# Kernel tuning notes

Measured on AMD Instinct MI355X. Metric: run time of the kernel, lower is better.

The kernel has to match this reference:

```python
import jax, jax.numpy as jnp
import numpy as np

EPS = 1e-5
GRID = (16, 16)
BLOCK = (16, 16)


def _ln(x):
    # LayerNorm over (C, H, W) per sample, affine = identity (fresh nn.LayerNorm each call)
    m = jnp.mean(x, axis=(1, 2, 3), keepdims=True)
    v = jnp.mean(jnp.square(x - m), axis=(1, 2, 3), keepdims=True)
    return (x - m) / jnp.sqrt(v + EPS)


def _gelu(x):
    return jax.nn.gelu(x, approximate=False)  # torch F.gelu default = exact erf


def _block(x, fh, fw):
    # NCHW -> [N, C, gh*gw, fh*fw]
    n, c, h, w = x.shape
    gh, gw = h // fh, w // fw
    return x.reshape(n, c, gh, fh, gw, fw).transpose(0, 1, 2, 4, 3, 5).reshape(n, c, gh * gw, fh * fw)


def _unblock(x, gh, gw, fh, fw):
    n, c, _, _ = x.shape
    return x.reshape(n, c, gh, gw, fh, fw).transpose(0, 1, 2, 4, 3, 5).reshape(n, c, gh * fh, gw * fw)


def _gating(x, w1, b1, w2, b2, w3, b3, w4, b4):
    # GetSpatialGatingWeights
    n, c, h, w = x.shape
    x = _ln(x)
    x = jnp.einsum('nchw,cd->ndhw', x, w1) + b1[None, :, None, None]  # C -> 2C
    x = _gelu(x)
    u, v = jnp.split(x, 2, axis=1)
    # grid MLP on u: mix across gh*gw grid positions
    gh, gw = GRID
    fh, fw = h // gh, w // gw
    u = _block(u, fh, fw)                                             # [n,c,G,P]
    u = jnp.einsum('ncgp,gd->ncdp', u, w2) + b2[None, None, :, None]
    u = _unblock(u, gh, gw, fh, fw)
    # block MLP on v: mix across fh*fw positions inside each block
    fh, fw = BLOCK
    gh, gw = h // fh, w // fw
    v = _block(v, fh, fw)
    v = jnp.einsum('ncgp,pd->ncgd', v, w3) + b3
    v = _unblock(v, gh, gw, fh, fw)
    x = jnp.concatenate([u, v], axis=1)
    return jnp.einsum('nchw,cd->ndhw', x, w4) + b4[None, :, None, None]  # 2C -> C


def _chan_lin(x, w, b):
    return jnp.einsum('nchw,cd->ndhw', x, w) + b[None, :, None, None]


def setup_inputs() -> dict:
    key = jax.random.key(0)
    ks = list(jax.random.split(key, 40))
    k = iter(ks)

    def rn(shape, s=0.02):
        return jax.random.normal(next(k), shape, dtype=jnp.float32) * s

    N, Cx, Cy, F, H, W = 8, 128, 256, 128, 128, 128
    G = GRID[0] * GRID[1]    # 256
    B = BLOCK[0] * BLOCK[1]  # 256
    inp = {
        'x': jax.random.normal(next(k), (N, Cx, H, W), dtype=jnp.float32),
        'y': jax.random.normal(next(k), (N, Cy, H // 2, W // 2), dtype=jnp.float32),
        'wt': rn((Cy, F, 2, 2)), 'bt': rn((F,)),
        'wc1': rn((Cx, F)), 'bc1': rn((F,)),
        'wc2': rn((F, F)), 'bc2': rn((F,)),
        'wl1': rn((F, F)), 'bl1': rn((F,)),
        'wl2': rn((F, F)), 'bl2': rn((F,)),
        'wl3': rn((F, F)), 'bl3': rn((F,)),
        'wl4': rn((F, F)), 'bl4': rn((F,)),
    }
    for p in ('g1', 'g2'):
        inp[p + '_w1'] = rn((F, 2 * F)); inp[p + '_b1'] = rn((2 * F,))
        inp[p + '_w2'] = rn((G, G));     inp[p + '_b2'] = rn((G,))
        inp[p + '_w3'] = rn((B, B));     inp[p + '_b3'] = rn((B,))
        inp[p + '_w4'] = rn((2 * F, F)); inp[p + '_b4'] = rn((F,))
    return inp


def reference(x, y, wt, bt, wc1, bc1, wc2, bc2, wl1, bl1, wl2, bl2, wl3, bl3, wl4, bl4,
              g1_w1, g1_b1, g1_w2, g1_b2, g1_w3, g1_b3, g1_w4, g1_b4,
              g2_w1, g2_b1, g2_w2, g2_b2, g2_w3, g2_b3, g2_w4, g2_b4):
    # ConvT_up: kernel=2, stride=2 (non-overlapping) + ReLU
    n, cy, hy, wy = y.shape
    fo = wt.shape[1]
    y = jnp.einsum('nchw,cokl->nohkwl', y, wt).reshape(n, fo, 2 * hy, 2 * wy) + bt[None, :, None, None]
    y = jax.nn.relu(y)
    # Conv1x1 (+ReLU) projections
    x = jax.nn.relu(_chan_lin(x, wc1, bc1))
    y = jax.nn.relu(_chan_lin(y, wc2, bc2))
    shortcut_x, shortcut_y = x, y
    # x branch
    x = _gelu(_chan_lin(_ln(x), wl1, bl1))
    gx = _gating(x, g1_w1, g1_b1, g1_w2, g1_b2, g1_w3, g1_b3, g1_w4, g1_b4)
    # y branch
    y = _gelu(_chan_lin(_ln(y), wl2, bl2))
    gy = _gating(y, g2_w1, g2_b1, g2_w2, g2_b2, g2_w3, g2_b3, g2_w4, g2_b4)
    # cross gating + residuals (dropout p=0.0 -> identity)
    y = _chan_lin(y * gx, wl3, bl3) + shortcut_y
    x = _chan_lin(x * gy, wl4, bl4) + y + shortcut_x
    return x, y
```

## Files before the change

### kernel.cpp

```cpp
#include <hip/hip_runtime.h>
#include <hip/hip_bf16.h>


typedef unsigned short u16;
typedef __bf16 bf16x8 __attribute__((ext_vector_type(8)));
typedef u16    u16x8  __attribute__((ext_vector_type(8)));
typedef u16    u16x4  __attribute__((ext_vector_type(4)));
typedef float  f32x4  __attribute__((ext_vector_type(4)));

__device__ __forceinline__ float bf2f(u16 u) {
  union { float f; unsigned int i; } v; v.i = ((unsigned int)u) << 16; return v.f;
}
__device__ __forceinline__ u16 f2bf(float f) {
  union { float f; unsigned int i; } v; v.f = f;
  unsigned int x = v.i;
  return (u16)((x + 0x7fffu + ((x >> 16) & 1u)) >> 16);
}
__device__ __forceinline__ f32x4 mfma16(u16x8 a, u16x8 b, f32x4 c) {
  return __builtin_amdgcn_mfma_f32_16x16x32_bf16(
      __builtin_bit_cast(bf16x8, a), __builtin_bit_cast(bf16x8, b), c, 0, 0, 0);
}
__device__ __forceinline__ float gelu_erf(float v) {
  return 0.5f * v * (1.0f + erff(v * 0.70710678118654752f));
}

__global__ __launch_bounds__(256) void prep_k(
    const float* __restrict__ wc1f, const float* __restrict__ wc2f,
    const float* __restrict__ wl1f, const float* __restrict__ wl2f,
    const float* __restrict__ wl3f, const float* __restrict__ wl4f,
    const float* __restrict__ g1w1, const float* __restrict__ g2w1,
    const float* __restrict__ g1w4, const float* __restrict__ g2w4,
    const float* __restrict__ g1w2, const float* __restrict__ g2w2,
    const float* __restrict__ g1w3, const float* __restrict__ g2w3,
    const float* __restrict__ wtf,
    u16* __restrict__ wb, float* __restrict__ cs, float* __restrict__ ps) {
  const int b = blockIdx.x, t = threadIdx.x;
  if (b < 384) {
    const float* src = b < 64 ? wc1f : b < 128 ? wc2f : b < 192 ? wl1f
                     : b < 256 ? wl2f : b < 320 ? wl3f : wl4f;
    const int w = b >> 6;
    const int i = ((b & 63) << 8) + t;
    const int d = i >> 7, c = i & 127;
    wb[w * 16384 + i] = f2bf(src[c * 128 + d]);
  } else if (b < 640) {
    const float* src = b < 512 ? g1w1 : g2w1;
    const int base = b < 512 ? 98304 : 131072;
    const int i = (((b - (b < 512 ? 384 : 512)) << 8) + t);
    const int d = i >> 7, c = i & 127;
    wb[base + i] = f2bf(src[c * 256 + d]);
  } else if (b < 896) {
    const float* src = b < 768 ? g1w4 : g2w4;
    const int base = b < 768 ? 163840 : 196608;
    const int i = (((b - (b < 768 ? 640 : 768)) << 8) + t);
    const int d = i >> 8, c = i & 255;
    wb[base + i] = f2bf(src[c * 128 + d]);
  } else if (b < 1920) {
    const int w = (b - 896) >> 8;
    const float* src = w == 0 ? g1w2 : w == 1 ? g2w2 : w == 2 ? g1w3 : g2w3;
    const int base = 229376 + w * 65536;
    const int i = (((b - 896) & 255) << 8) + t;
    const int d = i >> 8, g = i & 255;
    wb[base + i] = f2bf(src[g * 256 + d]);
  } else if (b < 2432) {
    const int i = ((b - 1920) << 8) + t;
    const int c = i & 255, r = i >> 8, o = r & 127, kl = r >> 7;
    wb[491520 + i] = f2bf(wtf[(c * 128 + o) * 4 + kl]);
  } else if (b < 2436) {
    const int w = b - 2432;
    const float* src = w == 0 ? wl1f : w == 1 ? wl2f : w == 2 ? g1w1 : g2w1;
    const int cout = w < 2 ? 128 : 256;
    if (t < cout) {
      float s = 0.f;
      for (int c = 0; c < 128; ++c) s += bf2f(f2bf(src[c * cout + t]));
      cs[w * 256 + t] = s;
    }
  } else {
    if (t < 64) ps[t] = 0.f;
  }
}

__global__ __launch_bounds__(256, 2) void gemmX_k(
    const float* __restrict__ X, const u16* __restrict__ Wt,
    const float* __restrict__ bias, u16* __restrict__ out,
    float* __restrict__ pso) {
  __shared__ u16 As[128 * 136];
  __shared__ float red[8];
  const int tid = threadIdx.x;
  const int m0 = blockIdx.x * 128;
  const int ns = m0 >> 14, pb = m0 & 16383;
  const int wid = tid >> 6, lane = tid & 63, fr = lane & 15, fg = lane >> 4;
  const int wmt = (wid & 1) * 64, wnc = (wid >> 1) * 64;

#pragma unroll
  for (int it = 0; it < 16; ++it) {
    const int idx = it * 256 + tid;
    const int c = idx & 127, t4 = idx >> 7;
    const f32x4 v = *(const f32x4*)(X + (((size_t)(ns * 128 + c)) << 14) + pb + t4 * 4);
#pragma unroll
    for (int r = 0; r < 4; ++r) As[(t4 * 4 + r) * 136 + c] = f2bf(v[r]);
  }
  __syncthreads();

  f32x4 acc[4][4] = {};
  const u16* Brow = Wt + (size_t)(wnc + fr) * 128;
  u16x8 a[4][4];
#pragma unroll
  for (int ks = 0; ks < 4; ++ks) {
    const int kb = ks * 32 + fg * 8;
#pragma unroll
    for (int i = 0; i < 4; ++i)
      a[ks][i] = *(const u16x8*)(As + (wmt + i * 16 + fr) * 136 + kb);
  }
#pragma unroll
  for (int ks = 0; ks < 4; ++ks) {
    const int kb = ks * 32 + fg * 8;
    u16x8 b_[4];
#pragma unroll
    for (int j = 0; j < 4; ++j)
      b_[j] = *(const u16x8*)(Brow + (size_t)j * 16 * 128 + kb);
#pragma unroll
    for (int i = 0; i < 4; ++i)
#pragma unroll
      for (int j = 0; j < 4; ++j) acc[i][j] = mfma16(b_[j], a[ks][i], acc[i][j]);
  }

  float s1 = 0.f, s2 = 0.f;
#pragma unroll
  for (int i = 0; i < 4; ++i) {
    const int token = m0 + wmt + i * 16 + fr;
#pragma unroll
    for (int j = 0; j < 4; ++j) {
      const int ch0 = wnc + j * 16 + fg * 4;
      const f32x4 bz = *(const f32x4*)(bias + ch0);
      f32x4 v = acc[i][j];
      u16x4 sv;
#pragma unroll
      for (int r = 0; r < 4; ++r) {
        v[r] = fmaxf(v[r] + bz[r], 0.f);
        s1 += v[r]; s2 += v[r] * v[r];
        sv[r] = f2bf(v[r]);
      }
      *(u16x4*)(out + (size_t)token * 128 + ch0) = sv;
    }
  }
#pragma unroll
  for (int off = 32; off > 0; off >>= 1) {
    s1 += __shfl_down(s1, off); s2 += __shfl_down(s2, off);
  }
  if (lane == 0) { red[wid] = s1; red[4 + wid] = s2; }
  __syncthreads();
  if (tid == 0)  atomicAdd(&pso[2 * ns],     red[0] + red[1] + red[2] + red[3]);
  if (tid == 64) atomicAdd(&pso[2 * ns + 1], red[4] + red[5] + red[6] + red[7]);
}

__global__ __launch_bounds__(256, 2) void gemmY_k(
    const float* __restrict__ Y, const u16* __restrict__ Wt,
    const float* __restrict__ bias, u16* __restrict__ out) {
  __shared__ u16 As[128 * 256];
  const int tid = threadIdx.x;
  const int m0 = blockIdx.x * 128;
  const int n0g = blockIdx.y * 128;
  const int ns = m0 >> 12, pb = m0 & 4095;
  const int wid = tid >> 6, lane = tid & 63, fr = lane & 15, fg = lane >> 4;
  const int wmt = (wid & 1) * 64, wnc = (wid >> 1) * 64;
  const int xorl = (fr & 7) << 4;

#pragma unroll
  for (int it = 0; it < 32; ++it) {
    const int idx = it * 256 + tid;
    const int c = idx & 255, t4 = idx >> 8;
    const f32x4 v = *(const f32x4*)(Y + (((size_t)(ns * 256 + c)) << 12) + pb + t4 * 4);
#pragma unroll
    for (int r = 0; r < 4; ++r) {
      const int tok = t4 * 4 + r;
      const int byte = (tok * 512 + c * 2) ^ ((tok & 7) << 4);
      *(u16*)((char*)As + byte) = f2bf(v[r]);
    }
  }
  __syncthreads();

  f32x4 acc[4][4] = {};
  const u16* Brow = Wt + (size_t)(n0g + wnc + fr) * 256;
#pragma unroll
  for (int h = 0; h < 2; ++h) {
    u16x8 a[4][4];
#pragma unroll
    for (int ks = 0; ks < 4; ++ks) {
      const int kb = (h * 4 + ks) * 32 + fg * 8;
#pragma unroll
      for (int i = 0; i < 4; ++i) {
        const int tok = wmt + i * 16 + fr;
        const int byte = (tok * 512 + kb * 2) ^ xorl;
        a[ks][i] = *(const u16x8*)((const char*)As + byte);
      }
    }
#pragma unroll
    for (int ks = 0; ks < 4; ++ks) {
      const int kb = (h * 4 + ks) * 32 + fg * 8;
      u16x8 b_[4];
#pragma unroll
      for (int j = 0; j < 4; ++j)
        b_[j] = *(const u16x8*)(Brow + (size_t)j * 16 * 256 + kb);
#pragma unroll
      for (int i = 0; i < 4; ++i)
#pragma unroll
        for (int j = 0; j < 4; ++j) acc[i][j] = mfma16(b_[j], a[ks][i], acc[i][j]);
    }
  }

#pragma unroll
  for (int i = 0; i < 4; ++i) {
    const int token = m0 + wmt + i * 16 + fr;
    const int nsY = token >> 12, hy = (token >> 6) & 63, wy = token & 63;
    const int kl = blockIdx.y;
    const int opix = ((nsY * 128 + 2 * hy + (kl >> 1)) << 7) + 2 * wy + (kl & 1);
#pragma unroll
    for (int j = 0; j < 4; ++j) {
      const int ch0 = wnc + j * 16 + fg * 4;
      const f32x4 bz = *(const f32x4*)(bias + ch0);
      u16x4 sv;
#pragma unroll
      for (int r = 0; r < 4; ++r) sv[r] = f2bf(fmaxf(acc[i][j][r] + bz[r], 0.f));
      *(u16x4*)(out + (size_t)opix * 128 + ch0) = sv;
    }
  }
}

template <int CIN, int LNF, int ACT, int STATS>
__global__ __launch_bounds__(256, 2) void gemm4_k(
    const u16* __restrict__ A1,
    const u16* __restrict__ Wt,
    const float* __restrict__ bias,
    const float* __restrict__ pst, const float* __restrict__ cs,
    u16* __restrict__ out,
    float* __restrict__ pso) {
  __shared__ float red[8];
  const int tid = threadIdx.x;
  const int m0 = blockIdx.x * 128;
  const int wid = tid >> 6, lane = tid & 63, fr = lane & 15, fg = lane >> 4;
  const int wmt = (wid & 1) * 64, wnc = (wid >> 1) * 64;

  f32x4 acc[4][4] = {};
  const u16* Arow = A1 + (size_t)(m0 + wmt + fr) * CIN;
  const u16* Brow = Wt + (size_t)(wnc + fr) * CIN;

  constexpr int NH = CIN / 128;
  u16x8 a[4][4];
#pragma unroll
  for (int h = 0; h < NH; ++h) {
#pragma unroll
    for (int ks = 0; ks < 4; ++ks) {
      const int kb = (h * 4 + ks) * 32 + fg * 8;
#pragma unroll
      for (int i = 0; i < 4; ++i)
        a[ks][i] = *(const u16x8*)(Arow + (size_t)i * 16 * CIN + kb);
    }
#pragma unroll
    for (int ks = 0; ks < 4; ++ks) {
      const int kb = (h * 4 + ks) * 32 + fg * 8;
      u16x8 b_[4];
#pragma unroll
      for (int j = 0; j < 4; ++j)
        b_[j] = *(const u16x8*)(Brow + (size_t)j * 16 * CIN + kb);
#pragma unroll
      for (int i = 0; i < 4; ++i)
#pragma unroll
        for (int j = 0; j < 4; ++j) acc[i][j] = mfma16(b_[j], a[ks][i], acc[i][j]);
    }
  }

  float alpha = 1.f, beta = 0.f;
  if constexpr (LNF) {
    const int s = m0 >> 14;
    const float inv_n = 1.f / 2097152.f;
    const float mean = pst[2 * s] * inv_n;
    const float var = pst[2 * s + 1] * inv_n - mean * mean;
    alpha = rsqrtf(var + 1e-5f);
    beta = -mean * alpha;
  }
  float s1 = 0.f, s2 = 0.f;
#pragma unroll
  for (int i = 0; i < 4; ++i) {
    const int token = m0 + wmt + i * 16 + fr;
#pragma unroll
    for (int j = 0; j < 4; ++j) {
      const int ch0 = wnc + j * 16 + fg * 4;
      const f32x4 bz = *(const f32x4*)(bias + ch0);
      f32x4 v = acc[i][j];
      if constexpr (LNF) {
        const f32x4 csv = *(const f32x4*)(cs + ch0);
#pragma unroll
        for (int r = 0; r < 4; ++r) v[r] = v[r] * alpha + beta * csv[r];
      }
      v += bz;
      if constexpr (ACT == 1) {
#pragma unroll
        for (int r = 0; r < 4; ++r) v[r] = fmaxf(v[r], 0.f);
      }
      if constexpr (ACT == 2) {
#pragma unroll
        for (int r = 0; r < 4; ++r) v[r] = gelu_erf(v[r]);
      }
      if constexpr (STATS) {
#pragma unroll
        for (int r = 0; r < 4; ++r) { s1 += v[r]; s2 += v[r] * v[r]; }
      }
      u16x4 sv;
#pragma unroll
      for (int r = 0; r < 4; ++r) sv[r] = f2bf(v[r]);
      *(u16x4*)(out + (size_t)token * 128 + ch0) = sv;
    }
  }
  if constexpr (STATS) {
#pragma unroll
    for (int off = 32; off > 0; off >>= 1) {
      s1 += __shfl_down(s1, off); s2 += __shfl_down(s2, off);
    }
    if (lane == 0) { red[wid] = s1; red[4 + wid] = s2; }
    __syncthreads();
    const int s = m0 >> 14;
    if (tid == 0)  atomicAdd(&pso[2 * s],     red[0] + red[1] + red[2] + red[3]);
    if (tid == 64) atomicAdd(&pso[2 * s + 1], red[4] + red[5] + red[6] + red[7]);
  }
}

template <int MODE>
__global__ __launch_bounds__(512, 2) void mlp3_k(
    const u16* __restrict__ y1, const u16* __restrict__ w1b,
    const float* __restrict__ b1, const float* __restrict__ pst,
    const float* __restrict__ csb,
    const u16* __restrict__ w2b, const float* __restrict__ b2,
    u16* __restrict__ uvout) {
  __shared__ u16 Ts[128 * 256];
  const int q2 = blockIdx.x, ns = blockIdx.y;
  const int tid = threadIdx.x;
  constexpr int coff = MODE ? 128 : 0;
  const int wid = tid >> 6, lane = tid & 63, fr = lane & 15, fg = lane >> 4;
  const int xorl = (fr & 7) << 4;

  int pbase, prow, pcol;
  if constexpr (MODE == 0) {
    pbase = ns * 16384 + (q2 >> 3) * 128 + (q2 & 7);
    prow = 1024; pcol = 8;
  } else {
    pbase = ns * 16384 + (q2 >> 3) * 2048 + (q2 & 7) * 16;
    prow = 128; pcol = 1;
  }
  auto pix = [&](int q) { return pbase + (q >> 4) * prow + (q & 15) * pcol; };

  {
    const int wgt = (wid >> 1) * 64;
    const int wc  = (wid & 1) * 64;
    const float inv_n = 1.f / 2097152.f;
    const float mean = pst[2 * ns] * inv_n;
    const float var = pst[2 * ns + 1] * inv_n - mean * mean;
    const float alpha = rsqrtf(var + 1e-5f);
    const float beta = -mean * alpha;

    f32x4 acc[4][4] = {};
    const u16* ar[4];
#pragma unroll
    for (int i = 0; i < 4; ++i)
      ar[i] = y1 + (size_t)pix(wgt + i * 16 + fr) * 128;
    const u16* br = w1b + (size_t)(coff + wc + fr) * 128;

    u16x8 a[4][4];
#pragma unroll
    for (int ks = 0; ks < 4; ++ks) {
      const int kb = ks * 32 + fg * 8;
#pragma unroll
      for (int i = 0; i < 4; ++i) a[ks][i] = *(const u16x8*)(ar[i] + kb);
    }
#pragma unroll
    for (int ks = 0; ks < 4; ++ks) {
      const int kb = ks * 32 + fg * 8;
      u16x8 b_[4];
#pragma unroll
      for (int j = 0; j < 4; ++j)
        b_[j] = *(const u16x8*)(br + (size_t)j * 16 * 128 + kb);
#pragma unroll
      for (int i = 0; i < 4; ++i)
#pragma unroll
        for (int j = 0; j < 4; ++j) acc[i][j] = mfma16(a[ks][i], b_[j], acc[i][j]);
    }
#pragma unroll
    for (int j = 0; j < 4; ++j) {
      const int c = wc + j * 16 + fr;
      const float cv = csb[coff + c];
      const float bz = b1[coff + c];
#pragma unroll
      for (int i = 0; i < 4; ++i) {
        const int g0 = wgt + i * 16 + fg * 4;
        u16x4 sv;
#pragma unroll
        for (int r = 0; r < 4; ++r)
          sv[r] = f2bf(gelu_erf(acc[i][j][r] * alpha + beta * cv + bz));
        const int byte = (c * 512 + g0 * 2) ^ xorl;
        *(u16x4*)((char*)Ts + byte) = sv;
      }
    }
  }
  __syncthreads();

  {
    const int wcs = (wid >> 2) * 64;
    const int wds = (wid & 3) * 64;
    f32x4 acc[4][4] = {};
    const u16* br = w2b + (size_t)(wds + fr) * 256;
#pragma unroll
    for (int h = 0; h < 2; ++h) {
      u16x8 a[4][4];
#pragma unroll
      for (int ks = 0; ks < 4; ++ks) {
        const int kb = (h * 4 + ks) * 32 + fg * 8;
#pragma unroll
        for (int i = 0; i < 4; ++i) {
          const int c = wcs + i * 16 + fr;
          const int byte = (c * 512 + kb * 2) ^ xorl;
          a[ks][i] = *(const u16x8*)((const char*)Ts + byte);
        }
      }
#pragma unroll
      for (int ks = 0; ks < 4; ++ks) {
        const int kb = (h * 4 + ks) * 32 + fg * 8;
        u16x8 b_[4];
#pragma unroll
        for (int j = 0; j < 4; ++j)
          b_[j] = *(const u16x8*)(br + (size_t)j * 16 * 256 + kb);
#pragma unroll
        for (int i = 0; i < 4; ++i)
#pragma unroll
          for (int j = 0; j < 4; ++j) acc[i][j] = mfma16(a[ks][i], b_[j], acc[i][j]);
      }
    }
#pragma unroll
    for (int j = 0; j < 4; ++j) {
      const int d = wds + j * 16 + fr;
      const float bz = b2[d];
      const size_t ob = (size_t)pix(d) * 256 + coff;
#pragma unroll
      for (int i = 0; i < 4; ++i) {
        const int c0 = wcs + i * 16 + fg * 4;
        u16x4 sv;
#pragma unroll
        for (int r = 0; r < 4; ++r) sv[r] = f2bf(acc[i][j][r] + bz);
        *(u16x4*)(uvout + ob + c0) = sv;
      }
    }
  }
}

__global__ __launch_bounds__(256, 2) void dual3_k(
    const u16* __restrict__ uv, const u16* __restrict__ g1w4b,
    const float* __restrict__ g1b4, const u16* __restrict__ y1,
    const u16* __restrict__ x1, const u16* __restrict__ gy,
    const u16* __restrict__ w3b, const u16* __restrict__ w4b,
    const float* __restrict__ b3, const float* __restrict__ b4,
    const u16* __restrict__ y0, const u16* __restrict__ x0,
    float* __restrict__ outy, float* __restrict__ outx) {
  __shared__ u16 Ls[128 * 136];
  const int tid = threadIdx.x;
  const int m0 = blockIdx.x * 128;
  const int wid = tid >> 6, lane = tid & 63, fr = lane & 15, fg = lane >> 4;
  const int wmt = (wid & 1) * 64, wnc = (wid >> 1) * 64;

  f32x4 acc[4][4] = {};
  u16x4 y9[4][4];

  {
    const u16* Arow = uv + (size_t)(m0 + wmt + fr) * 256;
    const u16* Brow = g1w4b + (size_t)(wnc + fr) * 256;
    u16x8 a[4][4];
#pragma unroll
    for (int h = 0; h < 2; ++h) {
#pragma unroll
      for (int ks = 0; ks < 4; ++ks) {
        const int kb = (h * 4 + ks) * 32 + fg * 8;
#pragma unroll
        for (int i = 0; i < 4; ++i)
          a[ks][i] = *(const u16x8*)(Arow + (size_t)i * 16 * 256 + kb);
      }
#pragma unroll
      for (int ks = 0; ks < 4; ++ks) {
        const int kb = (h * 4 + ks) * 32 + fg * 8;
        u16x8 b_[4];
#pragma unroll
        for (int j = 0; j < 4; ++j)
          b_[j] = *(const u16x8*)(Brow + (size_t)j * 16 * 256 + kb);
#pragma unroll
        for (int i = 0; i < 4; ++i)
#pragma unroll
          for (int j = 0; j < 4; ++j) acc[i][j] = mfma16(b_[j], a[ks][i], acc[i][j]);
      }
    }
    u16x4 mv[4][4];
#pragma unroll
    for (int i = 0; i < 4; ++i) {
      const int token = m0 + wmt + i * 16 + fr;
#pragma unroll
      for (int j = 0; j < 4; ++j)
        mv[i][j] = *(const u16x4*)(y1 + (size_t)token * 128 + wnc + j * 16 + fg * 4);
    }
#pragma unroll
    for (int i = 0; i < 4; ++i) {
      const int tok = wmt + i * 16 + fr;
#pragma unroll
      for (int j = 0; j < 4; ++j) {
        const int ch0 = wnc + j * 16 + fg * 4;
        const f32x4 bz = *(const f32x4*)(g1b4 + ch0);
        u16x4 sv;
#pragma unroll
        for (int r = 0; r < 4; ++r)
          sv[r] = f2bf((acc[i][j][r] + bz[r]) * bf2f(mv[i][j][r]));
        const int byte = (tok * 272 + ch0 * 2) ^ ((tok & 7) << 4);
        *(u16x4*)((char*)Ls + byte) = sv;
        acc[i][j] = f32x4{0.f, 0.f, 0.f, 0.f};
      }
    }
  }
  __syncthreads();

  {
    const u16* Brow = w3b + (size_t)(wnc + fr) * 128;
#pragma unroll
    for (int ks = 0; ks < 4; ++ks) {
      const int kb = ks * 32 + fg * 8;
      u16x8 a_[4], b_[4];
#pragma unroll
      for (int i = 0; i < 4; ++i) {
        const int tok = wmt + i * 16 + fr;
        const int byte = (tok * 272 + kb * 2) ^ ((tok & 7) << 4);
        a_[i] = *(const u16x8*)((const char*)Ls + byte);
      }
#pragma unroll
      for (int j = 0; j < 4; ++j) b_[j] = *(const u16x8*)(Brow + (size_t)j * 16 * 128 + kb);
#pragma unroll
      for (int i = 0; i < 4; ++i)
#pragma unroll
        for (int j = 0; j < 4; ++j) acc[i][j] = mfma16(b_[j], a_[i], acc[i][j]);
    }
  }
  {
    u16x4 scv[4][4];
#pragma unroll
    for (int i = 0; i < 4; ++i) {
      const int token = m0 + wmt + i * 16 + fr;
#pragma unroll
      for (int j = 0; j < 4; ++j)
        scv[i][j] = *(const u16x4*)(y0 + (size_t)token * 128 + wnc + j * 16 + fg * 4);
    }
#pragma unroll
    for (int i = 0; i < 4; ++i) {
      const int token = m0 + wmt + i * 16 + fr;
      const int ns = token >> 14, p = token & 16383;
#pragma unroll
      for (int j = 0; j < 4; ++j) {
        const int ch0 = wnc + j * 16 + fg * 4;
        const f32x4 bz = *(const f32x4*)(b3 + ch0);
        f32x4 v = acc[i][j];
#pragma unroll
        for (int r = 0; r < 4; ++r) {
          v[r] += bz[r] + bf2f(scv[i][j][r]);
          outy[((size_t)(ns * 128 + ch0 + r) << 14) + p] = v[r];
          y9[i][j][r] = f2bf(v[r]);
        }
        acc[i][j] = f32x4{0.f, 0.f, 0.f, 0.f};
      }
    }
  }
  {
    const u16* Arow  = x1 + (size_t)(m0 + wmt + fr) * 128;
    const u16* Arow2 = gy + (size_t)(m0 + wmt + fr) * 128;
    const u16* Brow  = w4b + (size_t)(wnc + fr) * 128;
    u16x8 a[4][4], a2[4][4];
#pragma unroll
    for (int ks = 0; ks < 4; ++ks) {
      const int kb = ks * 32 + fg * 8;
#pragma unroll
      for (int i = 0; i < 4; ++i) {
        a[ks][i]  = *(const u16x8*)(Arow  + (size_t)i * 16 * 128 + kb);
        a2[ks][i] = *(const u16x8*)(Arow2 + (size_t)i * 16 * 128 + kb);
      }
    }
#pragma unroll
    for (int ks = 0; ks < 4; ++ks) {
      const int kb = ks * 32 + fg * 8;
      u16x8 b_[4];
#pragma unroll
      for (int j = 0; j < 4; ++j) b_[j] = *(const u16x8*)(Brow + (size_t)j * 16 * 128 + kb);
      u16x8 am[4];
#pragma unroll
      for (int i = 0; i < 4; ++i) {
#pragma unroll
        for (int j = 0; j < 8; ++j) am[i][j] = f2bf(bf2f(a[ks][i][j]) * bf2f(a2[ks][i][j]));
      }
#pragma unroll
      for (int i = 0; i < 4; ++i)
#pragma unroll
        for (int j = 0; j < 4; ++j) acc[i][j] = mfma16(b_[j], am[i], acc[i][j]);
    }
  }
  {
    u16x4 scv[4][4];
#pragma unroll
    for (int i = 0; i < 4; ++i) {
      const int token = m0 + wmt + i * 16 + fr;
#pragma unroll
      for (int j = 0; j < 4; ++j)
        scv[i][j] = *(const u16x4*)(x0 + (size_t)token * 128 + wnc + j * 16 + fg * 4);
    }
#pragma unroll
    for (int i = 0; i < 4; ++i) {
      const int token = m0 + wmt + i * 16 + fr;
      const int ns = token >> 14, p = token & 16383;
#pragma unroll
      for (int j = 0; j < 4; ++j) {
        const int ch0 = wnc + j * 16 + fg * 4;
        const f32x4 bz = *(const f32x4*)(b4 + ch0);
        f32x4 v = acc[i][j];
#pragma unroll
        for (int r = 0; r < 4; ++r) {
          v[r] += bz[r] + bf2f(y9[i][j][r]) + bf2f(scv[i][j][r]);
          outx[((size_t)(ns * 128 + ch0 + r) << 14) + p] = v[r];
        }
      }
    }
  }
}

extern "C" void kernel_launch(void* const* d_in, const int* in_sizes, int n_in,
                              void* d_out, int out_size, void* d_ws, size_t ws_size,
                              hipStream_t stream) {
  (void)in_sizes; (void)n_in; (void)out_size; (void)ws_size;
  const float* xf   = (const float*)d_in[0];
  const float* yf   = (const float*)d_in[1];
  const float* wtf  = (const float*)d_in[2];
  const float* btf  = (const float*)d_in[3];
  const float* wc1f = (const float*)d_in[4];
  const float* bc1f = (const float*)d_in[5];
  const float* wc2f = (const float*)d_in[6];
  const float* bc2f = (const float*)d_in[7];
  const float* wl1f = (const float*)d_in[8];
  const float* bl1f = (const float*)d_in[9];
  const float* wl2f = (const float*)d_in[10];
  const float* bl2f = (const float*)d_in[11];
  const float* wl3f = (const float*)d_in[12];
  const float* bl3f = (const float*)d_in[13];
  const float* wl4f = (const float*)d_in[14];
  const float* bl4f = (const float*)d_in[15];
  const float* g1w1 = (const float*)d_in[16];
  const float* g1b1 = (const float*)d_in[17];
  const float* g1w2 = (const float*)d_in[18];
  const float* g1b2 = (const float*)d_in[19];
  const float* g1w3 = (const float*)d_in[20];
  const float* g1b3 = (const float*)d_in[21];
  const float* g1w4 = (const float*)d_in[22];
  const float* g1b4 = (const float*)d_in[23];
  const float* g2w1 = (const float*)d_in[24];
  const float* g2b1 = (const float*)d_in[25];
  const float* g2w2 = (const float*)d_in[26];
  const float* g2b2 = (const float*)d_in[27];
  const float* g2w3 = (const float*)d_in[28];
  const float* g2b3 = (const float*)d_in[29];
  const float* g2w4 = (const float*)d_in[30];
  const float* g2b4 = (const float*)d_in[31];

  constexpr int T16 = 16777216;
  u16* WS  = (u16*)d_ws;
  u16* x0b = WS;
  u16* x1b = WS + (size_t)T16;
  u16* y0b = WS + (size_t)2 * T16;
  u16* y1b = WS + (size_t)3 * T16;
  u16* gyb = WS + (size_t)4 * T16;
  u16* uvb = WS + (size_t)5 * T16;
  float* fb = (float*)(WS + (size_t)7 * T16);
  float* cs = fb;
  float* ps = fb + 1024;
  u16* wb   = (u16*)(fb + 1024 + 64);
  float* ps0 = ps, *ps1 = ps + 16, *ps2 = ps + 32, *ps3 = ps + 48;

  const u16* wc1b = wb;
  const u16* wc2b = wb + 16384;
  const u16* wl1b = wb + 32768;
  const u16* wl2b = wb + 49152;
  const u16* wl3b = wb + 65536;
  const u16* wl4b = wb + 81920;
  const u16* g1w1b = wb + 98304;
  const u16* g2w1b = wb + 131072;
  const u16* g1w4b = wb + 163840;
  const u16* g2w4b = wb + 196608;
  const u16* g1w2b = wb + 229376;
  const u16* g2w2b = wb + 294912;
  const u16* g1w3b = wb + 360448;
  const u16* g2w3b = wb + 425984;
  const u16* wtb   = wb + 491520;

  u16* tb    = (u16*)d_out;
  float* outx = (float*)d_out;
  float* outy = (float*)d_out + (size_t)T16;

  const dim3 B256(256), B512(512);

  prep_k<<<dim3(2437), B256, 0, stream>>>(
      wc1f, wc2f, wl1f, wl2f, wl3f, wl4f, g1w1, g2w1, g1w4, g2w4,
      g1w2, g2w2, g1w3, g2w3, wtf, wb, cs, ps);

  gemmY_k<<<dim3(256, 4), B256, 0, stream>>>(yf, wtb, btf, tb);
  gemmX_k<<<dim3(1024), B256, 0, stream>>>(xf, wc1b, bc1f, x0b, ps0);
  gemm4_k<128, 0, 1, 1><<<dim3(1024), B256, 0, stream>>>(
      tb, wc2b, bc2f, nullptr, nullptr, y0b, ps1);

  gemm4_k<128, 1, 2, 1><<<dim3(1024), B256, 0, stream>>>(
      y0b, wl2b, bl2f, ps1, cs + 256, y1b, ps3);
  mlp3_k<0><<<dim3(64, 8), B512, 0, stream>>>(
      y1b, g2w1b, g2b1, ps3, cs + 768, g2w2b, g2b2, uvb);
  mlp3_k<1><<<dim3(64, 8), B512, 0, stream>>>(
      y1b, g2w1b, g2b1, ps3, cs + 768, g2w3b, g2b3, uvb);
  gemm4_k<256, 0, 0, 0><<<dim3(1024), B256, 0, stream>>>(
      uvb, g2w4b, g2b4, nullptr, nullptr, gyb, nullptr);

  gemm4_k<128, 1, 2, 1><<<dim3(1024), B256, 0, stream>>>(
      x0b, wl1b, bl1f, ps0, cs, x1b, ps2);
  mlp3_k<0><<<dim3(64, 8), B512, 0, stream>>>(
      x1b, g1w1b, g1b1, ps2, cs + 512, g1w2b, g1b2, uvb);
  mlp3_k<1><<<dim3(64, 8), B512, 0, stream>>>(
      x1b, g1w1b, g1b1, ps2, cs + 512, g1w3b, g1b3, uvb);

  dual3_k<<<dim3(1024), B256, 0, stream>>>(
      uvb, g1w4b, g1b4, y1b, x1b, gyb, wl3b, wl4b, bl3f, bl4f,
      y0b, x0b, outy, outx);
}
```

Before: 611.2 us.

## Fuse ConvT with conv1x1 projection and fold w4 projection into gating MLP kernels

The transposed-conv GEMM is fused with the following 1x1 conv, ReLU and LayerNorm statistics, so the intermediate upsampled tensor stays in shared memory instead of going through global memory. Each gating MLP kernel now applies its half of the 2C->C w4 projection directly from shared memory. The second half accumulates into the bf16 output of the first, which removes the 256-channel uv buffer and a separate GEMM launch. The final dual kernel then reads the precomputed gx instead of recomputing the w4 GEMM. The cost is extra bf16 rounding of the partial gating sums, more shared memory per block, and a serial dependency between the two mlp3b launches.

Result: faster. 570.6 us (-6.6%).

```diff
diff --git a/kernel.cpp b/kernel.cpp
--- a/kernel.cpp
+++ b/kernel.cpp
@@ -153,20 +153,24 @@
   if (tid == 64) atomicAdd(&pso[2 * ns + 1], red[4] + red[5] + red[6] + red[7]);
 }
 
-__global__ __launch_bounds__(256, 2) void gemmY_k(
-    const float* __restrict__ Y, const u16* __restrict__ Wt,
-    const float* __restrict__ bias, u16* __restrict__ out) {
-  __shared__ u16 As[128 * 256];
+__global__ __launch_bounds__(256, 2) void gemmY2_k(
+    const float* __restrict__ Y, const u16* __restrict__ Wtb,
+    const float* __restrict__ bt, const u16* __restrict__ Wc2,
+    const float* __restrict__ bc2, u16* __restrict__ out,
+    float* __restrict__ pso) {
+  __shared__ u16 As[64 * 256];
+  __shared__ u16 Cs[64 * 136];
+  __shared__ float red[8];
   const int tid = threadIdx.x;
-  const int m0 = blockIdx.x * 128;
-  const int n0g = blockIdx.y * 128;
+  const int m0 = blockIdx.x * 64;
   const int ns = m0 >> 12, pb = m0 & 4095;
   const int wid = tid >> 6, lane = tid & 63, fr = lane & 15, fg = lane >> 4;
-  const int wmt = (wid & 1) * 64, wnc = (wid >> 1) * 64;
+  const int tokg = (wid & 1) * 32;
+  const int chg  = (wid >> 1) * 64;
   const int xorl = (fr & 7) << 4;
 
 #pragma unroll
-  for (int it = 0; it < 32; ++it) {
+  for (int it = 0; it < 16; ++it) {
     const int idx = it * 256 + tid;
     const int c = idx & 255, t4 = idx >> 8;
     const f32x4 v = *(const f32x4*)(Y + (((size_t)(ns * 256 + c)) << 12) + pb + t4 * 4);
@@ -179,61 +183,100 @@
   }
   __syncthreads();
 
-  f32x4 acc[4][4] = {};
-  const u16* Brow = Wt + (size_t)(n0g + wnc + fr) * 256;
-#pragma unroll
-  for (int h = 0; h < 2; ++h) {
-    u16x8 a[4][4];
-#pragma unroll
-    for (int ks = 0; ks < 4; ++ks) {
-      const int kb = (h * 4 + ks) * 32 + fg * 8;
-#pragma unroll
-      for (int i = 0; i < 4; ++i) {
-        const int tok = wmt + i * 16 + fr;
-        const int byte = (tok * 512 + kb * 2) ^ xorl;
-        a[ks][i] = *(const u16x8*)((const char*)As + byte);
-      }
-    }
-#pragma unroll
-    for (int ks = 0; ks < 4; ++ks) {
-      const int kb = (h * 4 + ks) * 32 + fg * 8;
-      u16x8 b_[4];
-#pragma unroll
-      for (int j = 0; j < 4; ++j)
-        b_[j] = *(const u16x8*)(Brow + (size_t)j * 16 * 256 + kb);
-#pragma unroll
-      for (int i = 0; i < 4; ++i)
-#pragma unroll
-        for (int j = 0; j < 4; ++j) acc[i][j] = mfma16(b_[j], a[ks][i], acc[i][j]);
-    }
-  }
-
-#pragma unroll
-  for (int i = 0; i < 4; ++i) {
-    const int token = m0 + wmt + i * 16 + fr;
-    const int nsY = token >> 12, hy = (token >> 6) & 63, wy = token & 63;
-    const int kl = blockIdx.y;
-    const int opix = ((nsY * 128 + 2 * hy + (kl >> 1)) << 7) + 2 * wy + (kl & 1);
-#pragma unroll
-    for (int j = 0; j < 4; ++j) {
-      const int ch0 = wnc + j * 16 + fg * 4;
-      const f32x4 bz = *(const f32x4*)(bias + ch0);
-      u16x4 sv;
-#pragma unroll
-      for (int r = 0; r < 4; ++r) sv[r] = f2bf(fmaxf(acc[i][j][r] + bz[r], 0.f));
-      *(u16x4*)(out + (size_t)opix * 128 + ch0) = sv;
-    }
-  }
-}
-
-template <int CIN, int LNF, int ACT, int STATS>
+  float s1 = 0.f, s2 = 0.f;
+  for (int kl = 0; kl < 4; ++kl) {
+    if (kl) __syncthreads();
+    f32x4 acc1[2][4] = {};
+    {
+      const u16* Brow = Wtb + (size_t)(kl * 128 + chg + fr) * 256;
+#pragma unroll
+      for (int ks = 0; ks < 8; ++ks) {
+        const int kb = ks * 32 + fg * 8;
+        u16x8 a_[2], b_[4];
+#pragma unroll
+        for (int i = 0; i < 2; ++i) {
+          const int tok = tokg + i * 16 + fr;
+          const int byte = (tok * 512 + kb * 2) ^ xorl;
+          a_[i] = *(const u16x8*)((const char*)As + byte);
+        }
+#pragma unroll
+        for (int j = 0; j < 4; ++j)
+          b_[j] = *(const u16x8*)(Brow + (size_t)j * 16 * 256 + kb);
+#pragma unroll
+        for (int i = 0; i < 2; ++i)
+#pragma unroll
+          for (int j = 0; j < 4; ++j) acc1[i][j] = mfma16(b_[j], a_[i], acc1[i][j]);
+      }
+    }
+#pragma unroll
+    for (int i = 0; i < 2; ++i) {
+      const int tok = tokg + i * 16 + fr;
+#pragma unroll
+      for (int j = 0; j < 4; ++j) {
+        const int o0 = chg + j * 16 + fg * 4;
+        const f32x4 bz = *(const f32x4*)(bt + o0);
+        u16x4 sv;
+#pragma unroll
+        for (int r = 0; r < 4; ++r) sv[r] = f2bf(fmaxf(acc1[i][j][r] + bz[r], 0.f));
+        *(u16x4*)(Cs + tok * 136 + o0) = sv;
+      }
+    }
+    __syncthreads();
+    f32x4 acc2[2][4] = {};
+    {
+      const u16* Brow = Wc2 + (size_t)(chg + fr) * 128;
+#pragma unroll
+      for (int ks = 0; ks < 4; ++ks) {
+        const int kb = ks * 32 + fg * 8;
+        u16x8 a_[2], b_[4];
+#pragma unroll
+        for (int i = 0; i < 2; ++i)
+          a_[i] = *(const u16x8*)(Cs + (tokg + i * 16 + fr) * 136 + kb);
+#pragma unroll
+        for (int j = 0; j < 4; ++j)
+          b_[j] = *(const u16x8*)(Brow + (size_t)j * 16 * 128 + kb);
+#pragma unroll
+        for (int i = 0; i < 2; ++i)
+#pragma unroll
+          for (int j = 0; j < 4; ++j) acc2[i][j] = mfma16(b_[j], a_[i], acc2[i][j]);
+      }
+    }
+#pragma unroll
+    for (int i = 0; i < 2; ++i) {
+      const int ytok = m0 + tokg + i * 16 + fr;
+      const int hy = (ytok >> 6) & 63, wy = ytok & 63;
+      const int opix = ((ns * 128 + 2 * hy + (kl >> 1)) << 7) + 2 * wy + (kl & 1);
+#pragma unroll
+      for (int j = 0; j < 4; ++j) {
+        const int ch0 = chg + j * 16 + fg * 4;
+        const f32x4 bz = *(const f32x4*)(bc2 + ch0);
+        u16x4 sv;
+#pragma unroll
+        for (int r = 0; r < 4; ++r) {
+          float v = fmaxf(acc2[i][j][r] + bz[r], 0.f);
+          s1 += v; s2 += v * v;
+          sv[r] = f2bf(v);
+        }
+        *(u16x4*)(out + (size_t)opix * 128 + ch0) = sv;
+      }
+    }
+  }
+#pragma unroll
+  for (int off = 32; off > 0; off >>= 1) {
+    s1 += __shfl_down(s1, off); s2 += __shfl_down(s2, off);
+  }
+  if (lane == 0) { red[wid] = s1; red[4 + wid] = s2; }
+  __syncthreads();
+  if (tid == 0)  atomicAdd(&pso[2 * ns],     red[0] + red[1] + red[2] + red[3]);
+  if (tid == 64) atomicAdd(&pso[2 * ns + 1], red[4] + red[5] + red[6] + red[7]);
+}
+
+template <int LNF>
 __global__ __launch_bounds__(256, 2) void gemm4_k(
-    const u16* __restrict__ A1,
-    const u16* __restrict__ Wt,
+    const u16* __restrict__ A1, const u16* __restrict__ Wt,
     const float* __restrict__ bias,
     const float* __restrict__ pst, const float* __restrict__ cs,
-    u16* __restrict__ out,
-    float* __restrict__ pso) {
+    u16* __restrict__ out, float* __restrict__ pso) {
   __shared__ float red[8];
   const int tid = threadIdx.x;
   const int m0 = blockIdx.x * 128;
@@ -241,32 +284,28 @@
   const int wmt = (wid & 1) * 64, wnc = (wid >> 1) * 64;
 
   f32x4 acc[4][4] = {};
-  const u16* Arow = A1 + (size_t)(m0 + wmt + fr) * CIN;
-  const u16* Brow = Wt + (size_t)(wnc + fr) * CIN;
-
-  constexpr int NH = CIN / 128;
+  const u16* Arow = A1 + (size_t)(m0 + wmt + fr) * 128;
+  const u16* Brow = Wt + (size_t)(wnc + fr) * 128;
+
   u16x8 a[4][4];
 #pragma unroll
-  for (int h = 0; h < NH; ++h) {
-#pragma unroll
-    for (int ks = 0; ks < 4; ++ks) {
-      const int kb = (h * 4 + ks) * 32 + fg * 8;
-#pragma unroll
-      for (int i = 0; i < 4; ++i)
-        a[ks][i] = *(const u16x8*)(Arow + (size_t)i * 16 * CIN + kb);
-    }
-#pragma unroll
-    for (int ks = 0; ks < 4; ++ks) {
-      const int kb = (h * 4 + ks) * 32 + fg * 8;
-      u16x8 b_[4];
-#pragma unroll
-      for (int j = 0; j < 4; ++j)
-        b_[j] = *(const u16x8*)(Brow + (size_t)j * 16 * CIN + kb);
-#pragma unroll
-      for (int i = 0; i < 4; ++i)
-#pragma unroll
-        for (int j = 0; j < 4; ++j) acc[i][j] = mfma16(b_[j], a[ks][i], acc[i][j]);
-    }
+  for (int ks = 0; ks < 4; ++ks) {
+    const int kb = ks * 32 + fg * 8;
+#pragma unroll
+    for (int i = 0; i < 4; ++i)
+      a[ks][i] = *(const u16x8*)(Arow + (size_t)i * 16 * 128 + kb);
+  }
+#pragma unroll
+  for (int ks = 0; ks < 4; ++ks) {
+    const int kb = ks * 32 + fg * 8;
+    u16x8 b_[4];
+#pragma unroll
+    for (int j = 0; j < 4; ++j)
+      b_[j] = *(const u16x8*)(Brow + (size_t)j * 16 * 128 + kb);
+#pragma unroll
+    for (int i = 0; i < 4; ++i)
+#pragma unroll
+      for (int j = 0; j < 4; ++j) acc[i][j] = mfma16(b_[j], a[ks][i], acc[i][j]);
   }
 
   float alpha = 1.f, beta = 0.f;
@@ -286,52 +325,39 @@
     for (int j = 0; j < 4; ++j) {
       const int ch0 = wnc + j * 16 + fg * 4;
       const f32x4 bz = *(const f32x4*)(bias + ch0);
+      const f32x4 csv = *(const f32x4*)(cs + ch0);
       f32x4 v = acc[i][j];
-      if constexpr (LNF) {
-        const f32x4 csv = *(const f32x4*)(cs + ch0);
-#pragma unroll
-        for (int r = 0; r < 4; ++r) v[r] = v[r] * alpha + beta * csv[r];
-      }
-      v += bz;
-      if constexpr (ACT == 1) {
-#pragma unroll
-        for (int r = 0; r < 4; ++r) v[r] = fmaxf(v[r], 0.f);
-      }
-      if constexpr (ACT == 2) {
-#pragma unroll
-        for (int r = 0; r < 4; ++r) v[r] = gelu_erf(v[r]);
-      }
-      if constexpr (STATS) {
-#pragma unroll
-        for (int r = 0; r < 4; ++r) { s1 += v[r]; s2 += v[r] * v[r]; }
-      }
       u16x4 sv;
 #pragma unroll
-      for (int r = 0; r < 4; ++r) sv[r] = f2bf(v[r]);
+      for (int r = 0; r < 4; ++r) {
+        v[r] = v[r] * alpha + beta * csv[r] + bz[r];
+        v[r] = gelu_erf(v[r]);
+        s1 += v[r]; s2 += v[r] * v[r];
+        sv[r] = f2bf(v[r]);
+      }
       *(u16x4*)(out + (size_t)token * 128 + ch0) = sv;
     }
   }
-  if constexpr (STATS) {
-#pragma unroll
-    for (int off = 32; off > 0; off >>= 1) {
-      s1 += __shfl_down(s1, off); s2 += __shfl_down(s2, off);
-    }
-    if (lane == 0) { red[wid] = s1; red[4 + wid] = s2; }
-    __syncthreads();
-    const int s = m0 >> 14;
-    if (tid == 0)  atomicAdd(&pso[2 * s],     red[0] + red[1] + red[2] + red[3]);
-    if (tid == 64) atomicAdd(&pso[2 * s + 1], red[4] + red[5] + red[6] + red[7]);
-  }
+#pragma unroll
+  for (int off = 32; off > 0; off >>= 1) {
+    s1 += __shfl_down(s1, off); s2 += __shfl_down(s2, off);
+  }
+  if (lane == 0) { red[wid] = s1; red[4 + wid] = s2; }
+  __syncthreads();
+  const int s = m0 >> 14;
+  if (tid == 0)  atomicAdd(&pso[2 * s],     red[0] + red[1] + red[2] + red[3]);
+  if (tid == 64) atomicAdd(&pso[2 * s + 1], red[4] + red[5] + red[6] + red[7]);
 }
 
 template <int MODE>
-__global__ __launch_bounds__(512, 2) void mlp3_k(
+__global__ __launch_bounds__(512, 2) void mlp3b_k(
     const u16* __restrict__ y1, const u16* __restrict__ w1b,
     const float* __restrict__ b1, const float* __restrict__ pst,
     const float* __restrict__ csb,
     const u16* __restrict__ w2b, const float* __restrict__ b2,
-    u16* __restrict__ uvout) {
-  __shared__ u16 Ts[128 * 256];
+    const u16* __restrict__ w4b, const float* __restrict__ b4,
+    u16* __restrict__ gout) {
+  __shared__ u16 Ts[34816];
   const int q2 = blockIdx.x, ns = blockIdx.y;
   const int tid = threadIdx.x;
   constexpr int coff = MODE ? 128 : 0;
@@ -402,10 +428,14 @@
   }
   __syncthreads();
 
+  f32x4 accB[4][4];
+  const int wcs = (wid >> 2) * 64;
+  const int wds = (wid & 3) * 64;
   {
-    const int wcs = (wid >> 2) * 64;
-    const int wds = (wid & 3) * 64;
-    f32x4 acc[4][4] = {};
+#pragma unroll
+    for (int i = 0; i < 4; ++i)
+#pragma unroll
+      for (int j = 0; j < 4; ++j) accB[i][j] = f32x4{0.f, 0.f, 0.f, 0.f};
     const u16* br = w2b + (size_t)(wds + fr) * 256;
 #pragma unroll
     for (int h = 0; h < 2; ++h) {
@@ -430,35 +460,77 @@
 #pragma unroll
         for (int i = 0; i < 4; ++i)
 #pragma unroll
-          for (int j = 0; j < 4; ++j) acc[i][j] = mfma16(a[ks][i], b_[j], acc[i][j]);
-      }
-    }
-#pragma unroll
-    for (int j = 0; j < 4; ++j) {
-      const int d = wds + j * 16 + fr;
-      const float bz = b2[d];
-      const size_t ob = (size_t)pix(d) * 256 + coff;
-#pragma unroll
-      for (int i = 0; i < 4; ++i) {
-        const int c0 = wcs + i * 16 + fg * 4;
+          for (int j = 0; j < 4; ++j) accB[i][j] = mfma16(a[ks][i], b_[j], accB[i][j]);
+      }
+    }
+  }
+  __syncthreads();
+
+#pragma unroll
+  for (int j = 0; j < 4; ++j) {
+    const int d = wds + j * 16 + fr;
+    const float bz = b2[d];
+#pragma unroll
+    for (int i = 0; i < 4; ++i) {
+      const int c0 = wcs + i * 16 + fg * 4;
+      u16x4 sv;
+#pragma unroll
+      for (int r = 0; r < 4; ++r) sv[r] = f2bf(accB[i][j][r] + bz);
+      *(u16x4*)(Ts + d * 136 + c0) = sv;
+    }
+  }
+  __syncthreads();
+
+  {
+    const int wp = (wid >> 1) * 64;
+    const int wo = (wid & 1) * 64;
+    f32x4 accC[4][4] = {};
+    const u16* br = w4b + (size_t)(wo + fr) * 256 + coff;
+#pragma unroll
+    for (int ks = 0; ks < 4; ++ks) {
+      const int kb = ks * 32 + fg * 8;
+      u16x8 a_[4], b_[4];
+#pragma unroll
+      for (int i = 0; i < 4; ++i)
+        a_[i] = *(const u16x8*)(Ts + (wp + i * 16 + fr) * 136 + kb);
+#pragma unroll
+      for (int j = 0; j < 4; ++j)
+        b_[j] = *(const u16x8*)(br + (size_t)j * 16 * 256 + kb);
+#pragma unroll
+      for (int i = 0; i < 4; ++i)
+#pragma unroll
+        for (int j = 0; j < 4; ++j) accC[i][j] = mfma16(b_[j], a_[i], accC[i][j]);
+    }
+#pragma unroll
+    for (int i = 0; i < 4; ++i) {
+      const size_t pg = (size_t)pix(wp + i * 16 + fr) * 128;
+#pragma unroll
+      for (int j = 0; j < 4; ++j) {
+        const int o0 = wo + j * 16 + fg * 4;
+        f32x4 v = accC[i][j];
         u16x4 sv;
-#pragma unroll
-        for (int r = 0; r < 4; ++r) sv[r] = f2bf(acc[i][j][r] + bz);
-        *(u16x4*)(uvout + ob + c0) = sv;
-      }
-    }
-  }
-}
-
-__global__ __launch_bounds__(256, 2) void dual3_k(
-    const u16* __restrict__ uv, const u16* __restrict__ g1w4b,
-    const float* __restrict__ g1b4, const u16* __restrict__ y1,
+        if constexpr (MODE == 0) {
+          const f32x4 bz = *(const f32x4*)(b4 + o0);
+#pragma unroll
+          for (int r = 0; r < 4; ++r) sv[r] = f2bf(v[r] + bz[r]);
+        } else {
+          const u16x4 pv = *(const u16x4*)(gout + pg + o0);
+#pragma unroll
+          for (int r = 0; r < 4; ++r) sv[r] = f2bf(v[r] + bf2f(pv[r]));
+        }
+        *(u16x4*)(gout + pg + o0) = sv;
+      }
+    }
+  }
+}
+
+__global__ __launch_bounds__(256, 2) void dual5_k(
+    const u16* __restrict__ y1, const u16* __restrict__ gx,
     const u16* __restrict__ x1, const u16* __restrict__ gy,
     const u16* __restrict__ w3b, const u16* __restrict__ w4b,
     const float* __restrict__ b3, const float* __restrict__ b4,
     const u16* __restrict__ y0, const u16* __restrict__ x0,
     float* __restrict__ outy, float* __restrict__ outx) {
-  __shared__ u16 Ls[128 * 136];
   const int tid = threadIdx.x;
   const int m0 = blockIdx.x * 128;
   const int wid = tid >> 6, lane = tid & 63, fr = lane & 15, fg = lane >> 4;
@@ -468,76 +540,34 @@
   u16x4 y9[4][4];
 
   {
-    const u16* Arow = uv + (size_t)(m0 + wmt + fr) * 256;
-    const u16* Brow = g1w4b + (size_t)(wnc + fr) * 256;
-    u16x8 a[4][4];
-#pragma unroll
-    for (int h = 0; h < 2; ++h) {
-#pragma unroll
-      for (int ks = 0; ks < 4; ++ks) {
-        const int kb = (h * 4 + ks) * 32 + fg * 8;
-#pragma unroll
-        for (int i = 0; i < 4; ++i)
-          a[ks][i] = *(const u16x8*)(Arow + (size_t)i * 16 * 256 + kb);
-      }
-#pragma unroll
-      for (int ks = 0; ks < 4; ++ks) {
-        const int kb = (h * 4 + ks) * 32 + fg * 8;
-        u16x8 b_[4];
-#pragma unroll
-        for (int j = 0; j < 4; ++j)
-          b_[j] = *(const u16x8*)(Brow + (size_t)j * 16 * 256 + kb);
-#pragma unroll
-        for (int i = 0; i < 4; ++i)
-#pragma unroll
-          for (int j = 0; j < 4; ++j) acc[i][j] = mfma16(b_[j], a[ks][i], acc[i][j]);
-      }
-    }
-    u16x4 mv[4][4];
-#pragma unroll
-    for (int i = 0; i < 4; ++i) {
-      const int token = m0 + wmt + i * 16 + fr;
-#pragma unroll
-      for (int j = 0; j < 4; ++j)
-        mv[i][j] = *(const u16x4*)(y1 + (size_t)token * 128 + wnc + j * 16 + fg * 4);
-    }
-#pragma unroll
-    for (int i = 0; i < 4; ++i) {
-      const int tok = wmt + i * 16 + fr;
-#pragma unroll
-      for (int j = 0; j < 4; ++j) {
-        const int ch0 = wnc + j * 16 + fg * 4;
-        const f32x4 bz = *(const f32x4*)(g1b4 + ch0);
-        u16x4 sv;
-#pragma unroll
-        for (int r = 0; r < 4; ++r)
-          sv[r] = f2bf((acc[i][j][r] + bz[r]) * bf2f(mv[i][j][r]));
-        const int byte = (tok * 272 + ch0 * 2) ^ ((tok & 7) << 4);
-        *(u16x4*)((char*)Ls + byte) = sv;
-        acc[i][j] = f32x4{0.f, 0.f, 0.f, 0.f};
-      }
-    }
-  }
-  __syncthreads();
-
-  {
-    const u16* Brow = w3b + (size_t)(wnc + fr) * 128;
+    const u16* Arow  = y1 + (size_t)(m0 + wmt + fr) * 128;
+    const u16* Arow2 = gx + (size_t)(m0 + wmt + fr) * 128;
+    const u16* Brow  = w3b + (size_t)(wnc + fr) * 128;
+    u16x8 a[4][4], a2[4][4];
 #pragma unroll
     for (int ks = 0; ks < 4; ++ks) {
       const int kb = ks * 32 + fg * 8;
-      u16x8 a_[4], b_[4];
 #pragma unroll
       for (int i = 0; i < 4; ++i) {
-        const int tok = wmt + i * 16 + fr;
-        const int byte = (tok * 272 + kb * 2) ^ ((tok & 7) << 4);
-        a_[i] = *(const u16x8*)((const char*)Ls + byte);
-      }
+        a[ks][i]  = *(const u16x8*)(Arow  + (size_t)i * 16 * 128 + kb);
+        a2[ks][i] = *(const u16x8*)(Arow2 + (size_t)i * 16 * 128 + kb);
+      }
+    }
+#pragma unroll
+    for (int ks = 0; ks < 4; ++ks) {
+      const int kb = ks * 32 + fg * 8;
+      u16x8 b_[4];
 #pragma unroll
       for (int j = 0; j < 4; ++j) b_[j] = *(const u16x8*)(Brow + (size_t)j * 16 * 128 + kb);
+      u16x8 am[4];
 #pragma unroll
       for (int i = 0; i < 4; ++i)
 #pragma unroll
-        for (int j = 0; j < 4; ++j) acc[i][j] = mfma16(b_[j], a_[i], acc[i][j]);
+        for (int j = 0; j < 8; ++j) am[i][j] = f2bf(bf2f(a[ks][i][j]) * bf2f(a2[ks][i][j]));
+#pragma unroll
+      for (int i = 0; i < 4; ++i)
+#pragma unroll
+        for (int j = 0; j < 4; ++j) acc[i][j] = mfma16(b_[j], am[i], acc[i][j]);
     }
   }
   {
@@ -590,10 +620,9 @@
       for (int j = 0; j < 4; ++j) b_[j] = *(const u16x8*)(Brow + (size_t)j * 16 * 128 + kb);
       u16x8 am[4];
 #pragma unroll
-      for (int i = 0; i < 4; ++i) {
+      for (int i = 0; i < 4; ++i)
 #pragma unroll
         for (int j = 0; j < 8; ++j) am[i][j] = f2bf(bf2f(a[ks][i][j]) * bf2f(a2[ks][i][j]));
-      }
 #pragma unroll
       for (int i = 0; i < 4; ++i)
 #pragma unroll
@@ -672,8 +701,8 @@
   u16* y0b = WS + (size_t)2 * T16;
   u16* y1b = WS + (size_t)3 * T16;
   u16* gyb = WS + (size_t)4 * T16;
-  u16* uvb = WS + (size_t)5 * T16;
-  float* fb = (float*)(WS + (size_t)7 * T16);
+  u16* gxb = WS + (size_t)5 * T16;
+  float* fb = (float*)(WS + (size_t)6 * T16);
   float* cs = fb;
   float* ps = fb + 1024;
   u16* wb   = (u16*)(fb + 1024 + 64);
@@ -695,7 +724,6 @@
   const u16* g2w3b = wb + 425984;
   const u16* wtb   = wb + 491520;
 
-  u16* tb    = (u16*)d_out;
   float* outx = (float*)d_out;
   float* outy = (float*)d_out + (size_t)T16;
 
@@ -705,28 +733,23 @@
       wc1f, wc2f, wl1f, wl2f, wl3f, wl4f, g1w1, g2w1, g1w4, g2w4,
       g1w2, g2w2, g1w3, g2w3, wtf, wb, cs, ps);
 
-  gemmY_k<<<dim3(256, 4), B256, 0, stream>>>(yf, wtb, btf, tb);
+  gemmY2_k<<<dim3(512), B256, 0, stream>>>(yf, wtb, btf, wc2b, bc2f, y0b, ps1);
   gemmX_k<<<dim3(1024), B256, 0, stream>>>(xf, wc1b, bc1f, x0b, ps0);
-  gemm4_k<128, 0, 1, 1><<<dim3(1024), B256, 0, stream>>>(
-      tb, wc2b, bc2f, nullptr, nullptr, y0b, ps1);
-
-  gemm4_k<128, 1, 2, 1><<<dim3(1024), B256, 0, stream>>>(
+
+  gemm4_k<1><<<dim3(1024), B256, 0, stream>>>(
       y0b, wl2b, bl2f, ps1, cs + 256, y1b, ps3);
-  mlp3_k<0><<<dim3(64, 8), B512, 0, stream>>>(
-      y1b, g2w1b, g2b1, ps3, cs + 768, g2w2b, g2b2, uvb);
-  mlp3_k<1><<<dim3(64, 8), B512, 0, stream>>>(
-      y1b, g2w1b, g2b1, ps3, cs + 768, g2w3b, g2b3, uvb);
-  gemm4_k<256, 0, 0, 0><<<dim3(1024), B256, 0, stream>>>(
-      uvb, g2w4b, g2b4, nullptr, nullptr, gyb, nullptr);
-
-  gemm4_k<128, 1, 2, 1><<<dim3(1024), B256, 0, stream>>>(
+  mlp3b_k<0><<<dim3(64, 8), B512, 0, stream>>>(
+      y1b, g2w1b, g2b1, ps3, cs + 768, g2w2b, g2b2, g2w4b, g2b4, gyb);
+  mlp3b_k<1><<<dim3(64, 8), B512, 0, stream>>>(
+      y1b, g2w1b, g2b1, ps3, cs + 768, g2w3b, g2b3, g2w4b, g2b4, gyb);
+
+  gemm4_k<1><<<dim3(1024), B256, 0, stream>>>(
       x0b, wl1b, bl1f, ps0, cs, x1b, ps2);
-  mlp3_k<0><<<dim3(64, 8), B512, 0, stream>>>(
-      x1b, g1w1b, g1b1, ps2, cs + 512, g1w2b, g1b2, uvb);
-  mlp3_k<1><<<dim3(64, 8), B512, 0, stream>>>(
-      x1b, g1w1b, g1b1, ps2, cs + 512, g1w3b, g1b3, uvb);
-
-  dual3_k<<<dim3(1024), B256, 0, stream>>>(
-      uvb, g1w4b, g1b4, y1b, x1b, gyb, wl3b, wl4b, bl3f, bl4f,
-      y0b, x0b, outy, outx);
-}
+  mlp3b_k<0><<<dim3(64, 8), B512, 0, stream>>>(
+      x1b, g1w1b, g1b1, ps2, cs + 512, g1w2b, g1b2, g1w4b, g1b4, gxb);
+  mlp3b_k<1><<<dim3(64, 8), B512, 0, stream>>>(
+      x1b, g1w1b, g1b1, ps2, cs + 512, g1w3b, g1b3, g1w4b, g1b4, gxb);
+
+  dual5_k<<<dim3(1024), B256, 0, stream>>>(
+      y1b, gxb, x1b, gyb, wl3b, wl4b, bl3f, bl4f, y0b, x0b, outy, outx);
+}
```
